# Performance work log

Hardware: AMD Instinct MI355X
Metric: run time of the kernel (lower is better)

## Reference

```python
import jax, jax.numpy as jnp
import numpy as np

B, D_MODEL, L = 4, 1024, 2048
D_STATE, D_CONV, EXPAND = 16, 4, 2
D_INNER = EXPAND * D_MODEL
DT_RANK = (D_MODEL + 15) // 16  # 64


def setup_inputs() -> dict:
    key = jax.random.key(0)
    ks = jax.random.split(key, 12)
    s = 0.02
    x = jax.random.normal(ks[0], (B, D_MODEL, L), dtype=jnp.float32)
    in_proj_w = jax.random.normal(ks[1], (2 * D_INNER, D_MODEL), dtype=jnp.float32) * s
    conv_w = jax.random.normal(ks[2], (D_INNER, D_CONV), dtype=jnp.float32) * 0.2
    conv_b = jnp.zeros((D_INNER,), dtype=jnp.float32)
    x_proj_w = jax.random.normal(ks[3], (DT_RANK + 2 * D_STATE, D_INNER), dtype=jnp.float32) * s
    dt_proj_w = jax.random.normal(ks[4], (D_INNER, DT_RANK), dtype=jnp.float32) * (DT_RANK ** -0.5)
    # bias init so softplus(bias) ~ dt in [1e-3, 1e-1], as in mamba_ssm
    dt = jnp.exp(jax.random.uniform(ks[5], (D_INNER,), dtype=jnp.float32)
                 * (np.log(0.1) - np.log(1e-3)) + np.log(1e-3))
    dt_proj_b = dt + jnp.log(-jnp.expm1(-dt))  # inverse softplus
    A_log = jnp.log(jnp.broadcast_to(jnp.arange(1, D_STATE + 1, dtype=jnp.float32),
                                     (D_INNER, D_STATE)))
    D = jnp.ones((D_INNER,), dtype=jnp.float32)
    out_proj_w = jax.random.normal(ks[6], (D_MODEL, D_INNER), dtype=jnp.float32) * s
    proj_w = jax.random.normal(ks[7], (D_MODEL, D_MODEL), dtype=jnp.float32) * s
    proj_b = jnp.zeros((D_MODEL,), dtype=jnp.float32)
    return dict(x=x, in_proj_w=in_proj_w, conv_w=conv_w, conv_b=conv_b,
                x_proj_w=x_proj_w, dt_proj_w=dt_proj_w, dt_proj_b=dt_proj_b,
                A_log=A_log, D=D, out_proj_w=out_proj_w, proj_w=proj_w, proj_b=proj_b)


def _mamba_forward(x, in_proj_w, conv_w, conv_b, x_proj_w, dt_proj_w, dt_proj_b,
                   A_log, D, out_proj_w, proj_w, proj_b):
    xt = jnp.transpose(x, (0, 2, 1))                      # (B, L, d_model)
    xz = jnp.einsum('bld,ed->ble', xt, in_proj_w)         # (B, L, 2*d_inner)
    u, z = jnp.split(xz, 2, axis=-1)                      # each (B, L, d_inner)

    # depthwise causal conv1d along time
    uc = jnp.transpose(u, (0, 2, 1))                      # (B, d_inner, L)
    upad = jnp.pad(uc, ((0, 0), (0, 0), (D_CONV - 1, 0)))
    conv = sum(conv_w[None, :, k, None] * upad[:, :, k:k + L] for k in range(D_CONV))
    conv = conv + conv_b[None, :, None]
    u = jax.nn.silu(jnp.transpose(conv, (0, 2, 1)))       # (B, L, d_inner)

    x_dbl = jnp.einsum('bld,ed->ble', u, x_proj_w)        # (B, L, dt_rank+2n)
    dt_low, Bm, Cm = jnp.split(x_dbl, [DT_RANK, DT_RANK + D_STATE], axis=-1)
    delta = jax.nn.softplus(jnp.einsum('blr,dr->bld', dt_low, dt_proj_w) + dt_proj_b)
    A = -jnp.exp(A_log)                                   # (d_inner, d_state)

    def step(h, inp):
        d_t, B_t, C_t, u_t = inp                          # (B,d),(B,n),(B,n),(B,d)
        dA = jnp.exp(d_t[:, :, None] * A[None])           # (B, d, n)
        dBu = d_t[:, :, None] * B_t[:, None, :] * u_t[:, :, None]
        h = dA * h + dBu
        y_t = jnp.einsum('bdn,bn->bd', h, C_t)
        return h, y_t

    xs = (jnp.transpose(delta, (1, 0, 2)), jnp.transpose(Bm, (1, 0, 2)),
          jnp.transpose(Cm, (1, 0, 2)), jnp.transpose(u, (1, 0, 2)))
    h0 = jnp.zeros((B, D_INNER, D_STATE), dtype=x.dtype)
    _, ys = jax.lax.scan(step, h0, xs)                    # ys: (L, B, d_inner)
    y = jnp.transpose(ys, (1, 0, 2)) + u * D              # (B, L, d_inner)
    y = y * jax.nn.silu(z)

    out = jnp.einsum('bld,ed->ble', y, out_proj_w)        # (B, L, d_model)
    out = jnp.einsum('bld,ed->ble', out, proj_w) + proj_b
    return jnp.transpose(out, (0, 2, 1))                  # (B, d_model, L)


def reference(x, in_proj_w, conv_w, conv_b, x_proj_w, dt_proj_w, dt_proj_b,
              A_log, D, out_proj_w, proj_w, proj_b):
    return _mamba_forward(x, in_proj_w, conv_w, conv_b, x_proj_w, dt_proj_w,
                          dt_proj_b, A_log, D, out_proj_w, proj_w, proj_b)
```

## Files before the change

kernel.cpp:

```cpp
#include <hip/hip_runtime.h>
#include <hip/hip_bf16.h>
#include <math.h>

#define BB 4
#define DMODEL 1024
#define LL 2048
#define DSTATE 16
#define DCONV 4
#define DINNER 2048
#define DTRANK 64
#define BL (BB * LL)
#define NCHUNK 32
#define LCH (LL / NCHUNK)
#define PFPLANE (BB * DINNER * DSTATE)
#define XPN 96
#define XPSPLIT 4
#define XPK (DINNER / XPSPLIT)

typedef unsigned short ushort;
typedef __bf16 bf16x8 __attribute__((ext_vector_type(8)));
typedef float f32x4 __attribute__((ext_vector_type(4)));

__device__ inline ushort f2bf(float f) {
    unsigned int u = __float_as_uint(f);
    u += 0x7fffu + ((u >> 16) & 1u);
    return (ushort)(u >> 16);
}
__device__ inline float bf2f(ushort h) {
    return __uint_as_float(((unsigned int)h) << 16);
}
__device__ inline float softplus_fast(float v) {
    float e = __expf(-fabsf(v));
    return fmaxf(v, 0.f) + __logf(1.f + e);
}

__device__ __forceinline__ void gload16(const ushort* g, ushort* l) {
    __builtin_amdgcn_global_load_lds(
        (__attribute__((address_space(1))) void*)g,
        (__attribute__((address_space(3))) void*)l, 16, 0, 0);
}

__global__ void f32_to_bf16(const float* __restrict__ src, ushort* __restrict__ dst, int n4) {
    int i = blockIdx.x * 256 + threadIdx.x;
    if (i < n4) {
        float4 v = ((const float4*)src)[i];
        ushort4 o;
        o.x = f2bf(v.x); o.y = f2bf(v.y); o.z = f2bf(v.z); o.w = f2bf(v.w);
        ((ushort4*)dst)[i] = o;
    }
}

__global__ void transpose_convert_x(const float* __restrict__ x, ushort* __restrict__ xtb) {
    __shared__ float tile[32][33];
    int b = blockIdx.z;
    int l0 = blockIdx.x * 32;
    int d0 = blockIdx.y * 32;
    int tx = threadIdx.x, ty = threadIdx.y;
    const float* xb = x + (size_t)b * DMODEL * LL;
#pragma unroll
    for (int j = 0; j < 32; j += 8)
        tile[ty + j][tx] = xb[(size_t)(d0 + ty + j) * LL + l0 + tx];
    __syncthreads();
    ushort* xtbb = xtb + (size_t)b * LL * DMODEL;
#pragma unroll
    for (int j = 0; j < 32; j += 8)
        xtbb[(size_t)(l0 + ty + j) * DMODEL + d0 + tx] = f2bf(tile[tx][ty + j]);
}

__global__ __launch_bounds__(256) void gemm_inproj(
    const ushort* __restrict__ A, const ushort* __restrict__ Bw,
    float* __restrict__ U, ushort* __restrict__ Z)
{
    __shared__ __align__(16) ushort As[128 * 32];
    __shared__ __align__(16) ushort Bs[128 * 32];
    const int tid = threadIdx.x;
    const int m0 = blockIdx.y * 128;
    const int n0 = blockIdx.x * 128;
    const int wave = tid >> 6;
    const int lane = tid & 63;
    const int wm = (wave >> 1) * 64;
    const int wn = (wave & 1) * 64;
    const int fr = lane & 15;
    const int fq = lane >> 4;
    const int fk = fq * 8;
    const int gr = lane >> 2;
    const int gc = (lane & 3) * 8;

    f32x4 acc[4][4];
#pragma unroll
    for (int i = 0; i < 4; ++i)
#pragma unroll
        for (int j = 0; j < 4; ++j)
            acc[i][j] = (f32x4)(0.0f);

    const ushort* Ag0 = A + (size_t)(m0 + wave * 16 + gr) * DMODEL + gc;
    const ushort* Ag1 = Ag0 + (size_t)64 * DMODEL;
    const ushort* Bg0 = Bw + (size_t)(n0 + wave * 16 + gr) * DMODEL + gc;
    const ushort* Bg1 = Bg0 + (size_t)64 * DMODEL;
    ushort* la0 = &As[wave * 512 + lane * 8];
    ushort* la1 = &As[(wave + 4) * 512 + lane * 8];
    ushort* lb0 = &Bs[wave * 512 + lane * 8];
    ushort* lb1 = &Bs[(wave + 4) * 512 + lane * 8];

    for (int k0 = 0; k0 < DMODEL; k0 += 32) {
        __syncthreads();
        gload16(Ag0 + k0, la0);
        gload16(Ag1 + k0, la1);
        gload16(Bg0 + k0, lb0);
        gload16(Bg1 + k0, lb1);
        __syncthreads();
        bf16x8 af[4], bfr[4];
#pragma unroll
        for (int i = 0; i < 4; ++i)
            af[i] = *(const bf16x8*)&As[(wm + i * 16 + fr) * 32 + fk];
#pragma unroll
        for (int j = 0; j < 4; ++j)
            bfr[j] = *(const bf16x8*)&Bs[(wn + j * 16 + fr) * 32 + fk];
#pragma unroll
        for (int i = 0; i < 4; ++i)
#pragma unroll
            for (int j = 0; j < 4; ++j)
                acc[i][j] = __builtin_amdgcn_mfma_f32_16x16x32_bf16(
                    af[i], bfr[j], acc[i][j], 0, 0, 0);
    }

    if (n0 < DINNER) {
#pragma unroll
        for (int i = 0; i < 4; ++i)
#pragma unroll
            for (int r = 0; r < 4; ++r) {
                int row = m0 + wm + i * 16 + fq * 4 + r;
#pragma unroll
                for (int j = 0; j < 4; ++j)
                    U[(size_t)row * DINNER + n0 + wn + j * 16 + fr] = acc[i][j][r];
            }
    } else {
#pragma unroll
        for (int i = 0; i < 4; ++i)
#pragma unroll
            for (int r = 0; r < 4; ++r) {
                int row = m0 + wm + i * 16 + fq * 4 + r;
#pragma unroll
                for (int j = 0; j < 4; ++j)
                    Z[(size_t)row * DINNER + (n0 - DINNER) + wn + j * 16 + fr] =
                        f2bf(acc[i][j][r]);
            }
    }
}

__global__ __launch_bounds__(256) void gemm_bf16(
    const ushort* __restrict__ A, const ushort* __restrict__ Bw,
    float* __restrict__ C, ushort* __restrict__ Cb,
    const float* __restrict__ bias,
    int M, int N, int K, int lda, int ldb, int ldc, int ldcb, int nbmax, int flags)
{
    __shared__ __align__(16) ushort As[128 * 32];
    __shared__ __align__(16) ushort Bs[128 * 32];
    const int tid = threadIdx.x;
    const int m0 = blockIdx.y * 128;
    const int n0 = blockIdx.x * 128;
    const int wave = tid >> 6;
    const int lane = tid & 63;
    const int wm = (wave >> 1) * 64;
    const int wn = (wave & 1) * 64;
    const int fr = lane & 15;
    const int fq = lane >> 4;
    const int fk = fq * 8;
    const int gr = lane >> 2;
    const int gc = (lane & 3) * 8;

    f32x4 acc[4][4];
#pragma unroll
    for (int i = 0; i < 4; ++i)
#pragma unroll
        for (int j = 0; j < 4; ++j)
            acc[i][j] = (f32x4)(0.0f);

    const ushort* Ag0 = A + (size_t)(m0 + wave * 16 + gr) * lda + gc;
    const ushort* Ag1 = Ag0 + (size_t)64 * lda;
    const ushort* Bg0 = Bw + (size_t)(n0 + wave * 16 + gr) * ldb + gc;
    const ushort* Bg1 = Bg0 + (size_t)64 * ldb;
    ushort* la0 = &As[wave * 512 + lane * 8];
    ushort* la1 = &As[(wave + 4) * 512 + lane * 8];
    ushort* lb0 = &Bs[wave * 512 + lane * 8];
    ushort* lb1 = &Bs[(wave + 4) * 512 + lane * 8];

    for (int k0 = 0; k0 < K; k0 += 32) {
        __syncthreads();
        gload16(Ag0 + k0, la0);
        gload16(Ag1 + k0, la1);
        gload16(Bg0 + k0, lb0);
        gload16(Bg1 + k0, lb1);
        __syncthreads();
        bf16x8 af[4], bfr[4];
#pragma unroll
        for (int i = 0; i < 4; ++i)
            af[i] = *(const bf16x8*)&As[(wm + i * 16 + fr) * 32 + fk];
#pragma unroll
        for (int j = 0; j < 4; ++j)
            bfr[j] = *(const bf16x8*)&Bs[(wn + j * 16 + fr) * 32 + fk];
#pragma unroll
        for (int i = 0; i < 4; ++i)
#pragma unroll
            for (int j = 0; j < 4; ++j)
                acc[i][j] = __builtin_amdgcn_mfma_f32_16x16x32_bf16(
                    af[i], bfr[j], acc[i][j], 0, 0, 0);
    }

#pragma unroll
    for (int i = 0; i < 4; ++i) {
#pragma unroll
        for (int r = 0; r < 4; ++r) {
            int row = m0 + wm + i * 16 + fq * 4 + r;
#pragma unroll
            for (int j = 0; j < 4; ++j) {
                int col = n0 + wn + j * 16 + fr;
                if (col < N) {
                    float v = acc[i][j][r];
                    if (flags & 4) v += bias[col];
                    if (flags & 8) v = softplus_fast(v);
                    if (flags & 1) C[(size_t)row * ldc + col] = v;
                    if ((flags & 2) && col < nbmax)
                        Cb[(size_t)row * ldcb + col] = f2bf(v);
                }
            }
        }
    }
}

__global__ __launch_bounds__(256) void gemm_xproj(
    const ushort* __restrict__ A, const ushort* __restrict__ Bw,
    float* __restrict__ Pp)
{
    __shared__ __align__(16) ushort As[128 * 32];
    __shared__ __align__(16) ushort Bs[128 * 32];
    const int tid = threadIdx.x;
    const int kp = blockIdx.x;
    const int m0 = blockIdx.y * 128;
    const int kbase = kp * XPK;
    const int wave = tid >> 6;
    const int lane = tid & 63;
    const int wm = (wave >> 1) * 64;
    const int wn = (wave & 1) * 64;
    const int fr = lane & 15;
    const int fq = lane >> 4;
    const int fk = fq * 8;
    const int gr = lane >> 2;
    const int gc = (lane & 3) * 8;

    f32x4 acc[4][4];
#pragma unroll
    for (int i = 0; i < 4; ++i)
#pragma unroll
        for (int j = 0; j < 4; ++j)
            acc[i][j] = (f32x4)(0.0f);

    const ushort* Ag0 = A + (size_t)(m0 + wave * 16 + gr) * DINNER + kbase + gc;
    const ushort* Ag1 = Ag0 + (size_t)64 * DINNER;
    const ushort* Bg0 = Bw + (size_t)(wave * 16 + gr) * DINNER + kbase + gc;
    const ushort* Bg1 = Bg0 + (size_t)64 * DINNER;
    ushort* la0 = &As[wave * 512 + lane * 8];
    ushort* la1 = &As[(wave + 4) * 512 + lane * 8];
    ushort* lb0 = &Bs[wave * 512 + lane * 8];
    ushort* lb1 = &Bs[(wave + 4) * 512 + lane * 8];

    for (int k0 = 0; k0 < XPK; k0 += 32) {
        __syncthreads();
        gload16(Ag0 + k0, la0);
        gload16(Ag1 + k0, la1);
        gload16(Bg0 + k0, lb0);
        gload16(Bg1 + k0, lb1);
        __syncthreads();
        bf16x8 af[4], bfr[4];
#pragma unroll
        for (int i = 0; i < 4; ++i)
            af[i] = *(const bf16x8*)&As[(wm + i * 16 + fr) * 32 + fk];
#pragma unroll
        for (int j = 0; j < 4; ++j)
            bfr[j] = *(const bf16x8*)&Bs[(wn + j * 16 + fr) * 32 + fk];
#pragma unroll
        for (int i = 0; i < 4; ++i)
#pragma unroll
            for (int j = 0; j < 4; ++j)
                acc[i][j] = __builtin_amdgcn_mfma_f32_16x16x32_bf16(
                    af[i], bfr[j], acc[i][j], 0, 0, 0);
    }

    float* Cp = Pp + (size_t)kp * ((size_t)BL * XPN);
#pragma unroll
    for (int i = 0; i < 4; ++i) {
#pragma unroll
        for (int r = 0; r < 4; ++r) {
            int row = m0 + wm + i * 16 + fq * 4 + r;
#pragma unroll
            for (int j = 0; j < 4; ++j) {
                int col = wn + j * 16 + fr;
                if (col < XPN)
                    Cp[(size_t)row * XPN + col] = acc[i][j][r];
            }
        }
    }
}

__global__ __launch_bounds__(256) void xproj_reduce(
    const float* __restrict__ Pp, float* __restrict__ xdbl, ushort* __restrict__ dtlow)
{
    int g = blockIdx.x * 256 + threadIdx.x;
    const size_t S = (size_t)BL * XPN;
    float s = (Pp[g] + Pp[g + S]) + (Pp[g + 2 * S] + Pp[g + 3 * S]);
    xdbl[g] = s;
    int row = g / XPN;
    int col = g - row * XPN;
    if (col < DTRANK) dtlow[row * DTRANK + col] = f2bf(s);
}

__global__ void conv_silu(const float* __restrict__ u, const float* __restrict__ cw,
                          const float* __restrict__ cb, ushort* __restrict__ ucb) {
    int idx = blockIdx.x * 256 + threadIdx.x;
    int d4 = idx & (DINNER / 4 - 1);
    int bl = idx >> 9;
    int l = bl & (LL - 1);
    int d = d4 << 2;
    const float* up = u + (size_t)bl * DINNER + d;
    const float4* cwv = (const float4*)cw;
    float4 w0 = cwv[d], w1 = cwv[d + 1], w2 = cwv[d + 2], w3 = cwv[d + 3];
    float4 bv = *(const float4*)(cb + d);
    float4 t = *(const float4*)(up);
    float4 a;
    a.x = fmaf(w0.w, t.x, bv.x);
    a.y = fmaf(w1.w, t.y, bv.y);
    a.z = fmaf(w2.w, t.z, bv.z);
    a.w = fmaf(w3.w, t.w, bv.w);
    if (l >= 1) {
        t = *(const float4*)(up - DINNER);
        a.x = fmaf(w0.z, t.x, a.x); a.y = fmaf(w1.z, t.y, a.y);
        a.z = fmaf(w2.z, t.z, a.z); a.w = fmaf(w3.z, t.w, a.w);
    }
    if (l >= 2) {
        t = *(const float4*)(up - 2 * DINNER);
        a.x = fmaf(w0.y, t.x, a.x); a.y = fmaf(w1.y, t.y, a.y);
        a.z = fmaf(w2.y, t.z, a.z); a.w = fmaf(w3.y, t.w, a.w);
    }
    if (l >= 3) {
        t = *(const float4*)(up - 3 * DINNER);
        a.x = fmaf(w0.x, t.x, a.x); a.y = fmaf(w1.x, t.y, a.y);
        a.z = fmaf(w2.x, t.z, a.z); a.w = fmaf(w3.x, t.w, a.w);
    }
    ushort4 o;
    o.x = f2bf(a.x / (1.f + __expf(-a.x)));
    o.y = f2bf(a.y / (1.f + __expf(-a.y)));
    o.z = f2bf(a.z / (1.f + __expf(-a.z)));
    o.w = f2bf(a.w / (1.f + __expf(-a.w)));
    ((ushort4*)ucb)[idx] = o;
}

__global__ __launch_bounds__(256) void scan_phase1(
    const ushort* __restrict__ delta16, const float* __restrict__ xdbl,
    const ushort* __restrict__ ucb, const float* __restrict__ A_log,
    float* __restrict__ P, float* __restrict__ F)
{
    int g = blockIdx.x * 256 + threadIdx.x;
    int d = g & (DINNER - 1);
    int c = (g >> 11) & (NCHUNK - 1);
    int b = g >> 16;

    float An[16], p[16], f[16];
    const float4* alp = (const float4*)(A_log + (size_t)d * DSTATE);
#pragma unroll
    for (int q = 0; q < 4; ++q) {
        float4 a = alp[q];
        An[q * 4 + 0] = -__expf(a.x); An[q * 4 + 1] = -__expf(a.y);
        An[q * 4 + 2] = -__expf(a.z); An[q * 4 + 3] = -__expf(a.w);
    }
#pragma unroll
    for (int n = 0; n < 16; ++n) { p[n] = 1.f; f[n] = 0.f; }

    size_t bl0 = (size_t)b * LL + (size_t)c * LCH;
    const ushort* dptr = delta16 + bl0 * DINNER + d;
    const ushort* uptr = ucb + bl0 * DINNER + d;
    const float* xptr = xdbl + bl0 * 96 + DTRANK;

#pragma unroll 2
    for (int l = 0; l < LCH; ++l) {
        float dv = bf2f(dptr[(size_t)l * DINNER]);
        float du = dv * bf2f(uptr[(size_t)l * DINNER]);
        float4 B0 = *(const float4*)(xptr + (size_t)l * 96);
        float4 B1 = *(const float4*)(xptr + (size_t)l * 96 + 4);
        float4 B2 = *(const float4*)(xptr + (size_t)l * 96 + 8);
        float4 B3 = *(const float4*)(xptr + (size_t)l * 96 + 12);
        float Bv[16] = {B0.x, B0.y, B0.z, B0.w, B1.x, B1.y, B1.z, B1.w,
                        B2.x, B2.y, B2.z, B2.w, B3.x, B3.y, B3.z, B3.w};
#pragma unroll
        for (int n = 0; n < 16; ++n) {
            float dA = __expf(dv * An[n]);
            f[n] = fmaf(dA, f[n], du * Bv[n]);
            p[n] *= dA;
        }
    }
    size_t o = (size_t)c * PFPLANE + ((size_t)(b * DINNER + d) << 4);
#pragma unroll
    for (int q = 0; q < 4; ++q) {
        *(float4*)(P + o + q * 4) = make_float4(p[q*4], p[q*4+1], p[q*4+2], p[q*4+3]);
        *(float4*)(F + o + q * 4) = make_float4(f[q*4], f[q*4+1], f[q*4+2], f[q*4+3]);
    }
}

__global__ __launch_bounds__(256) void scan_phase2(
    float* __restrict__ P, const float* __restrict__ F)
{
    int g = blockIdx.x * 256 + threadIdx.x;
    float h = 0.f;
#pragma unroll
    for (int c = 0; c < NCHUNK; ++c) {
        size_t idx = (size_t)c * PFPLANE + g;
        float pv = P[idx];
        float fv = F[idx];
        P[idx] = h;
        h = fmaf(pv, h, fv);
    }
}

__global__ __launch_bounds__(256) void scan_phase3(
    const ushort* __restrict__ delta16, const float* __restrict__ xdbl,
    const ushort* __restrict__ ucb, const ushort* __restrict__ zb,
    const float* __restrict__ A_log, const float* __restrict__ Dp,
    const float* __restrict__ Hin, ushort* __restrict__ ybf)
{
    int g = blockIdx.x * 256 + threadIdx.x;
    int d = g & (DINNER - 1);
    int c = (g >> 11) & (NCHUNK - 1);
    int b = g >> 16;

    float An[16], h[16];
    const float4* alp = (const float4*)(A_log + (size_t)d * DSTATE);
#pragma unroll
    for (int q = 0; q < 4; ++q) {
        float4 a = alp[q];
        An[q * 4 + 0] = -__expf(a.x); An[q * 4 + 1] = -__expf(a.y);
        An[q * 4 + 2] = -__expf(a.z); An[q * 4 + 3] = -__expf(a.w);
    }
    size_t o = (size_t)c * PFPLANE + ((size_t)(b * DINNER + d) << 4);
#pragma unroll
    for (int q = 0; q < 4; ++q) {
        float4 hv = *(const float4*)(Hin + o + q * 4);
        h[q * 4 + 0] = hv.x; h[q * 4 + 1] = hv.y;
        h[q * 4 + 2] = hv.z; h[q * 4 + 3] = hv.w;
    }
    float Dd = Dp[d];

    size_t bl0 = (size_t)b * LL + (size_t)c * LCH;
    const ushort* dptr = delta16 + bl0 * DINNER + d;
    const ushort* uptr = ucb + bl0 * DINNER + d;
    const ushort* zptr = zb + bl0 * DINNER + d;
    const float* xptr = xdbl + bl0 * 96 + DTRANK;
    ushort* yptr = ybf + bl0 * DINNER + d;

#pragma unroll 2
    for (int l = 0; l < LCH; ++l) {
        float dv = bf2f(dptr[(size_t)l * DINNER]);
        float uv = bf2f(uptr[(size_t)l * DINNER]);
        float zv = bf2f(zptr[(size_t)l * DINNER]);
        float du = dv * uv;
        float4 B0 = *(const float4*)(xptr + (size_t)l * 96);
        float4 B1 = *(const float4*)(xptr + (size_t)l * 96 + 4);
        float4 B2 = *(const float4*)(xptr + (size_t)l * 96 + 8);
        float4 B3 = *(const float4*)(xptr + (size_t)l * 96 + 12);
        float4 C0 = *(const float4*)(xptr + (size_t)l * 96 + 16);
        float4 C1 = *(const float4*)(xptr + (size_t)l * 96 + 20);
        float4 C2 = *(const float4*)(xptr + (size_t)l * 96 + 24);
        float4 C3 = *(const float4*)(xptr + (size_t)l * 96 + 28);
        float Bv[16] = {B0.x, B0.y, B0.z, B0.w, B1.x, B1.y, B1.z, B1.w,
                        B2.x, B2.y, B2.z, B2.w, B3.x, B3.y, B3.z, B3.w};
        float Cv[16] = {C0.x, C0.y, C0.z, C0.w, C1.x, C1.y, C1.z, C1.w,
                        C2.x, C2.y, C2.z, C2.w, C3.x, C3.y, C3.z, C3.w};
        float y0 = 0.f, y1 = 0.f, y2 = 0.f, y3 = 0.f;
#pragma unroll
        for (int n = 0; n < 4; ++n) {
            float dA0 = __expf(dv * An[n]);
            float dA1 = __expf(dv * An[n + 4]);
            float dA2 = __expf(dv * An[n + 8]);
            float dA3 = __expf(dv * An[n + 12]);
            h[n]      = fmaf(dA0, h[n],      du * Bv[n]);
            h[n + 4]  = fmaf(dA1, h[n + 4],  du * Bv[n + 4]);
            h[n + 8]  = fmaf(dA2, h[n + 8],  du * Bv[n + 8]);
            h[n + 12] = fmaf(dA3, h[n + 12], du * Bv[n + 12]);
            y0 = fmaf(h[n],      Cv[n],      y0);
            y1 = fmaf(h[n + 4],  Cv[n + 4],  y1);
            y2 = fmaf(h[n + 8],  Cv[n + 8],  y2);
            y3 = fmaf(h[n + 12], Cv[n + 12], y3);
        }
        float y = (y0 + y1) + (y2 + y3);
        float sz = zv / (1.f + __expf(-zv));
        yptr[(size_t)l * DINNER] = f2bf((y + uv * Dd) * sz);
    }
}

__global__ void transpose_out(const float* __restrict__ o2, float* __restrict__ out) {
    __shared__ float tile[32][33];
    int b = blockIdx.z;
    int l0 = blockIdx.x * 32;
    int e0 = blockIdx.y * 32;
    int tx = threadIdx.x, ty = threadIdx.y;
    const float* ob = o2 + (size_t)b * LL * DMODEL;
#pragma unroll
    for (int j = 0; j < 32; j += 8)
        tile[ty + j][tx] = ob[(size_t)(l0 + ty + j) * DMODEL + e0 + tx];
    __syncthreads();
    float* outb = out + (size_t)b * DMODEL * LL;
#pragma unroll
    for (int j = 0; j < 32; j += 8)
        outb[(size_t)(e0 + ty + j) * LL + l0 + tx] = tile[tx][ty + j];
}

extern "C" void kernel_launch(void* const* d_in, const int* in_sizes, int n_in,
                              void* d_out, int out_size, void* d_ws, size_t ws_size,
                              hipStream_t stream) {
    const float* x         = (const float*)d_in[0];
    const float* in_proj_w = (const float*)d_in[1];
    const float* conv_w    = (const float*)d_in[2];
    const float* conv_b    = (const float*)d_in[3];
    const float* x_proj_w  = (const float*)d_in[4];
    const float* dt_proj_w = (const float*)d_in[5];
    const float* dt_proj_b = (const float*)d_in[6];
    const float* A_log     = (const float*)d_in[7];
    const float* Dp        = (const float*)d_in[8];
    const float* out_proj_w= (const float*)d_in[9];
    const float* proj_w    = (const float*)d_in[10];
    const float* proj_b    = (const float*)d_in[11];
    float* out = (float*)d_out;

    char* wsb = (char*)d_ws;
    float*  bufU    = (float*)(wsb);
    ushort* delta16 = (ushort*)(wsb);
    float*  Pbuf    = (float*)(wsb + ((size_t)32 << 20));
    float*  xprojP  = (float*)(wsb + ((size_t)32 << 20));
    float*  Fbuf    = (float*)(wsb + ((size_t)48 << 20));
    ushort* zb      = (ushort*)(wsb + ((size_t)64 << 20));
    ushort* xtb     = (ushort*)(wsb + ((size_t)96 << 20));
    ushort* ucb     = (ushort*)(wsb + ((size_t)96 << 20));
    ushort* ybf     = (ushort*)(wsb + ((size_t)128 << 20));
    float*  xdbl    = (float*)(wsb + ((size_t)160 << 20));
    ushort* dtlow   = (ushort*)(wsb + ((size_t)163 << 20));
    ushort* wip     = (ushort*)(wsb + ((size_t)164 << 20));
    ushort* wxp     = wip + (size_t)4194304;
    ushort* wdt     = wxp + (size_t)196608;
    ushort* wop     = wdt + (size_t)131072;
    ushort* wpj     = wop + (size_t)2097152;
    float*  out2    = (float*)(wsb);
    ushort* out1b   = (ushort*)(wsb + ((size_t)32 << 20));

    f32_to_bf16<<<dim3(4096), 256, 0, stream>>>(in_proj_w, wip, 1048576);
    f32_to_bf16<<<dim3(192),  256, 0, stream>>>(x_proj_w,  wxp, 49152);
    f32_to_bf16<<<dim3(128),  256, 0, stream>>>(dt_proj_w, wdt, 32768);
    f32_to_bf16<<<dim3(2048), 256, 0, stream>>>(out_proj_w, wop, 524288);
    f32_to_bf16<<<dim3(1024), 256, 0, stream>>>(proj_w,    wpj, 262144);

    transpose_convert_x<<<dim3(LL / 32, DMODEL / 32, BB), dim3(32, 8), 0, stream>>>(x, xtb);

    gemm_inproj<<<dim3(2 * DINNER / 128, BL / 128), 256, 0, stream>>>(
        xtb, wip, bufU, zb);

    conv_silu<<<dim3(BL * DINNER / 4 / 256), 256, 0, stream>>>(bufU, conv_w, conv_b, ucb);

    gemm_xproj<<<dim3(XPSPLIT, BL / 128), 256, 0, stream>>>(ucb, wxp, xprojP);
    xproj_reduce<<<dim3(BL * XPN / 256), 256, 0, stream>>>(xprojP, xdbl, dtlow);

    gemm_bf16<<<dim3(DINNER / 128, BL / 128), 256, 0, stream>>>(
        dtlow, wdt, nullptr, delta16, dt_proj_b,
        BL, DINNER, DTRANK, DTRANK, DTRANK, 0, DINNER, DINNER, 2 | 4 | 8);

    const int scan_threads = BB * NCHUNK * DINNER;
    scan_phase1<<<dim3(scan_threads / 256), 256, 0, stream>>>(
        delta16, xdbl, ucb, A_log, Pbuf, Fbuf);
    scan_phase2<<<dim3(PFPLANE / 256), 256, 0, stream>>>(Pbuf, Fbuf);
    scan_phase3<<<dim3(scan_threads / 256), 256, 0, stream>>>(
        delta16, xdbl, ucb, zb, A_log, Dp, Pbuf, ybf);

    gemm_bf16<<<dim3(DMODEL / 128, BL / 128), 256, 0, stream>>>(
        ybf, wop, nullptr, out1b, nullptr,
        BL, DMODEL, DINNER, DINNER, DINNER, 0, DMODEL, DMODEL, 2);

    gemm_bf16<<<dim3(DMODEL / 128, BL / 128), 256, 0, stream>>>(
        out1b, wpj, out2, nullptr, proj_b,
        BL, DMODEL, DMODEL, DMODEL, DMODEL, DMODEL, 0, 0, 1 | 4);

    transpose_out<<<dim3(LL / 32, DMODEL / 32, BB), dim3(32, 8), 0, stream>>>(out2, out);
}
```

Before: 649.4 us.

## Double-buffer LDS in GEMMs and fuse output transpose into final projection

All three bf16 GEMM kernels now use two LDS buffers so the global-to-LDS load of the next k-tile is issued before the MFMAs on the current tile, with one barrier per iteration instead of two. The final projection GEMM is computed with swapped operands (weights times activations), so its epilogue writes directly into the (B, d_model, L) output layout with a per-row bias, and the separate transpose kernel and its intermediate buffer are removed. This doubles LDS usage per block, which may lower occupancy. The transposed-layout stores are strided along L per lane group and may coalesce less well.

```diff
diff --git a/kernel.cpp b/kernel.cpp
--- a/kernel.cpp
+++ b/kernel.cpp
@@ -67,12 +67,13 @@
         xtbb[(size_t)(l0 + ty + j) * DMODEL + d0 + tx] = f2bf(tile[tx][ty + j]);
 }
 
+
 __global__ __launch_bounds__(256) void gemm_inproj(
     const ushort* __restrict__ A, const ushort* __restrict__ Bw,
     float* __restrict__ U, ushort* __restrict__ Z)
 {
-    __shared__ __align__(16) ushort As[128 * 32];
-    __shared__ __align__(16) ushort Bs[128 * 32];
+    __shared__ __align__(16) ushort As[2][128 * 32];
+    __shared__ __align__(16) ushort Bs[2][128 * 32];
     const int tid = threadIdx.x;
     const int m0 = blockIdx.y * 128;
     const int n0 = blockIdx.x * 128;
@@ -97,31 +98,39 @@
     const ushort* Ag1 = Ag0 + (size_t)64 * DMODEL;
     const ushort* Bg0 = Bw + (size_t)(n0 + wave * 16 + gr) * DMODEL + gc;
     const ushort* Bg1 = Bg0 + (size_t)64 * DMODEL;
-    ushort* la0 = &As[wave * 512 + lane * 8];
-    ushort* la1 = &As[(wave + 4) * 512 + lane * 8];
-    ushort* lb0 = &Bs[wave * 512 + lane * 8];
-    ushort* lb1 = &Bs[(wave + 4) * 512 + lane * 8];
-
-    for (int k0 = 0; k0 < DMODEL; k0 += 32) {
-        __syncthreads();
-        gload16(Ag0 + k0, la0);
-        gload16(Ag1 + k0, la1);
-        gload16(Bg0 + k0, lb0);
-        gload16(Bg1 + k0, lb1);
-        __syncthreads();
+
+    auto stage = [&](int s, int k0) {
+        gload16(Ag0 + k0, &As[s][wave * 512 + lane * 8]);
+        gload16(Ag1 + k0, &As[s][(wave + 4) * 512 + lane * 8]);
+        gload16(Bg0 + k0, &Bs[s][wave * 512 + lane * 8]);
+        gload16(Bg1 + k0, &Bs[s][(wave + 4) * 512 + lane * 8]);
+    };
+
+    stage(0, 0);
+    asm volatile("s_waitcnt vmcnt(0)" ::: "memory");
+    __builtin_amdgcn_s_barrier();
+    asm volatile("" ::: "memory");
+
+    const int NT = DMODEL / 32;
+    for (int t = 0; t < NT; ++t) {
+        const int cur = t & 1;
+        if (t + 1 < NT) stage(cur ^ 1, (t + 1) * 32);
         bf16x8 af[4], bfr[4];
 #pragma unroll
         for (int i = 0; i < 4; ++i)
-            af[i] = *(const bf16x8*)&As[(wm + i * 16 + fr) * 32 + fk];
+            af[i] = *(const bf16x8*)&As[cur][(wm + i * 16 + fr) * 32 + fk];
 #pragma unroll
         for (int j = 0; j < 4; ++j)
-            bfr[j] = *(const bf16x8*)&Bs[(wn + j * 16 + fr) * 32 + fk];
+            bfr[j] = *(const bf16x8*)&Bs[cur][(wn + j * 16 + fr) * 32 + fk];
 #pragma unroll
         for (int i = 0; i < 4; ++i)
 #pragma unroll
             for (int j = 0; j < 4; ++j)
                 acc[i][j] = __builtin_amdgcn_mfma_f32_16x16x32_bf16(
                     af[i], bfr[j], acc[i][j], 0, 0, 0);
+        asm volatile("s_waitcnt vmcnt(0) lgkmcnt(0)" ::: "memory");
+        __builtin_amdgcn_s_barrier();
+        asm volatile("" ::: "memory");
     }
 
     if (n0 < DINNER) {
@@ -154,8 +163,8 @@
     const float* __restrict__ bias,
     int M, int N, int K, int lda, int ldb, int ldc, int ldcb, int nbmax, int flags)
 {
-    __shared__ __align__(16) ushort As[128 * 32];
-    __shared__ __align__(16) ushort Bs[128 * 32];
+    __shared__ __align__(16) ushort As[2][128 * 32];
+    __shared__ __align__(16) ushort Bs[2][128 * 32];
     const int tid = threadIdx.x;
     const int m0 = blockIdx.y * 128;
     const int n0 = blockIdx.x * 128;
@@ -180,31 +189,39 @@
     const ushort* Ag1 = Ag0 + (size_t)64 * lda;
     const ushort* Bg0 = Bw + (size_t)(n0 + wave * 16 + gr) * ldb + gc;
     const ushort* Bg1 = Bg0 + (size_t)64 * ldb;
-    ushort* la0 = &As[wave * 512 + lane * 8];
-    ushort* la1 = &As[(wave + 4) * 512 + lane * 8];
-    ushort* lb0 = &Bs[wave * 512 + lane * 8];
-    ushort* lb1 = &Bs[(wave + 4) * 512 + lane * 8];
-
-    for (int k0 = 0; k0 < K; k0 += 32) {
-        __syncthreads();
-        gload16(Ag0 + k0, la0);
-        gload16(Ag1 + k0, la1);
-        gload16(Bg0 + k0, lb0);
-        gload16(Bg1 + k0, lb1);
-        __syncthreads();
+
+    auto stage = [&](int s, int k0) {
+        gload16(Ag0 + k0, &As[s][wave * 512 + lane * 8]);
+        gload16(Ag1 + k0, &As[s][(wave + 4) * 512 + lane * 8]);
+        gload16(Bg0 + k0, &Bs[s][wave * 512 + lane * 8]);
+        gload16(Bg1 + k0, &Bs[s][(wave + 4) * 512 + lane * 8]);
+    };
+
+    stage(0, 0);
+    asm volatile("s_waitcnt vmcnt(0)" ::: "memory");
+    __builtin_amdgcn_s_barrier();
+    asm volatile("" ::: "memory");
+
+    const int NT = K / 32;
+    for (int t = 0; t < NT; ++t) {
+        const int cur = t & 1;
+        if (t + 1 < NT) stage(cur ^ 1, (t + 1) * 32);
         bf16x8 af[4], bfr[4];
 #pragma unroll
         for (int i = 0; i < 4; ++i)
-            af[i] = *(const bf16x8*)&As[(wm + i * 16 + fr) * 32 + fk];
+            af[i] = *(const bf16x8*)&As[cur][(wm + i * 16 + fr) * 32 + fk];
 #pragma unroll
         for (int j = 0; j < 4; ++j)
-            bfr[j] = *(const bf16x8*)&Bs[(wn + j * 16 + fr) * 32 + fk];
+            bfr[j] = *(const bf16x8*)&Bs[cur][(wn + j * 16 + fr) * 32 + fk];
 #pragma unroll
         for (int i = 0; i < 4; ++i)
 #pragma unroll
             for (int j = 0; j < 4; ++j)
                 acc[i][j] = __builtin_amdgcn_mfma_f32_16x16x32_bf16(
                     af[i], bfr[j], acc[i][j], 0, 0, 0);
+        asm volatile("s_waitcnt vmcnt(0) lgkmcnt(0)" ::: "memory");
+        __builtin_amdgcn_s_barrier();
+        asm volatile("" ::: "memory");
     }
 
 #pragma unroll
@@ -217,11 +234,18 @@
                 int col = n0 + wn + j * 16 + fr;
                 if (col < N) {
                     float v = acc[i][j][r];
-                    if (flags & 4) v += bias[col];
-                    if (flags & 8) v = softplus_fast(v);
-                    if (flags & 1) C[(size_t)row * ldc + col] = v;
-                    if ((flags & 2) && col < nbmax)
-                        Cb[(size_t)row * ldcb + col] = f2bf(v);
+                    if (flags & 16) {
+                        v += bias[row];
+                        int bq = col >> 11;
+                        int l  = col & (LL - 1);
+                        C[(size_t)bq * DMODEL * LL + (size_t)row * LL + l] = v;
+                    } else {
+                        if (flags & 4) v += bias[col];
+                        if (flags & 8) v = softplus_fast(v);
+                        if (flags & 1) C[(size_t)row * ldc + col] = v;
+                        if ((flags & 2) && col < nbmax)
+                            Cb[(size_t)row * ldcb + col] = f2bf(v);
+                    }
                 }
             }
         }
@@ -232,8 +256,8 @@
     const ushort* __restrict__ A, const ushort* __restrict__ Bw,
     float* __restrict__ Pp)
 {
-    __shared__ __align__(16) ushort As[128 * 32];
-    __shared__ __align__(16) ushort Bs[128 * 32];
+    __shared__ __align__(16) ushort As[2][128 * 32];
+    __shared__ __align__(16) ushort Bs[2][128 * 32];
     const int tid = threadIdx.x;
     const int kp = blockIdx.x;
     const int m0 = blockIdx.y * 128;
@@ -259,31 +283,39 @@
     const ushort* Ag1 = Ag0 + (size_t)64 * DINNER;
     const ushort* Bg0 = Bw + (size_t)(wave * 16 + gr) * DINNER + kbase + gc;
     const ushort* Bg1 = Bg0 + (size_t)64 * DINNER;
-    ushort* la0 = &As[wave * 512 + lane * 8];
-    ushort* la1 = &As[(wave + 4) * 512 + lane * 8];
-    ushort* lb0 = &Bs[wave * 512 + lane * 8];
-    ushort* lb1 = &Bs[(wave + 4) * 512 + lane * 8];
-
-    for (int k0 = 0; k0 < XPK; k0 += 32) {
-        __syncthreads();
-        gload16(Ag0 + k0, la0);
-        gload16(Ag1 + k0, la1);
-        gload16(Bg0 + k0, lb0);
-        gload16(Bg1 + k0, lb1);
-        __syncthreads();
+
+    auto stage = [&](int s, int k0) {
+        gload16(Ag0 + k0, &As[s][wave * 512 + lane * 8]);
+        gload16(Ag1 + k0, &As[s][(wave + 4) * 512 + lane * 8]);
+        gload16(Bg0 + k0, &Bs[s][wave * 512 + lane * 8]);
+        gload16(Bg1 + k0, &Bs[s][(wave + 4) * 512 + lane * 8]);
+    };
+
+    stage(0, 0);
+    asm volatile("s_waitcnt vmcnt(0)" ::: "memory");
+    __builtin_amdgcn_s_barrier();
+    asm volatile("" ::: "memory");
+
+    const int NT = XPK / 32;
+    for (int t = 0; t < NT; ++t) {
+        const int cur = t & 1;
+        if (t + 1 < NT) stage(cur ^ 1, (t + 1) * 32);
         bf16x8 af[4], bfr[4];
 #pragma unroll
         for (int i = 0; i < 4; ++i)
-            af[i] = *(const bf16x8*)&As[(wm + i * 16 + fr) * 32 + fk];
+            af[i] = *(const bf16x8*)&As[cur][(wm + i * 16 + fr) * 32 + fk];
 #pragma unroll
         for (int j = 0; j < 4; ++j)
-            bfr[j] = *(const bf16x8*)&Bs[(wn + j * 16 + fr) * 32 + fk];
+            bfr[j] = *(const bf16x8*)&Bs[cur][(wn + j * 16 + fr) * 32 + fk];
 #pragma unroll
         for (int i = 0; i < 4; ++i)
 #pragma unroll
             for (int j = 0; j < 4; ++j)
                 acc[i][j] = __builtin_amdgcn_mfma_f32_16x16x32_bf16(
                     af[i], bfr[j], acc[i][j], 0, 0, 0);
+        asm volatile("s_waitcnt vmcnt(0) lgkmcnt(0)" ::: "memory");
+        __builtin_amdgcn_s_barrier();
+        asm volatile("" ::: "memory");
     }
 
     float* Cp = Pp + (size_t)kp * ((size_t)BL * XPN);
@@ -495,23 +527,6 @@
     }
 }
 
-__global__ void transpose_out(const float* __restrict__ o2, float* __restrict__ out) {
-    __shared__ float tile[32][33];
-    int b = blockIdx.z;
-    int l0 = blockIdx.x * 32;
-    int e0 = blockIdx.y * 32;
-    int tx = threadIdx.x, ty = threadIdx.y;
-    const float* ob = o2 + (size_t)b * LL * DMODEL;
-#pragma unroll
-    for (int j = 0; j < 32; j += 8)
-        tile[ty + j][tx] = ob[(size_t)(l0 + ty + j) * DMODEL + e0 + tx];
-    __syncthreads();
-    float* outb = out + (size_t)b * DMODEL * LL;
-#pragma unroll
-    for (int j = 0; j < 32; j += 8)
-        outb[(size_t)(e0 + ty + j) * LL + l0 + tx] = tile[tx][ty + j];
-}
-
 extern "C" void kernel_launch(void* const* d_in, const int* in_sizes, int n_in,
                               void* d_out, int out_size, void* d_ws, size_t ws_size,
                               hipStream_t stream) {
@@ -546,7 +561,6 @@
     ushort* wdt     = wxp + (size_t)196608;
     ushort* wop     = wdt + (size_t)131072;
     ushort* wpj     = wop + (size_t)2097152;
-    float*  out2    = (float*)(wsb);
     ushort* out1b   = (ushort*)(wsb + ((size_t)32 << 20));
 
     f32_to_bf16<<<dim3(4096), 256, 0, stream>>>(in_proj_w, wip, 1048576);
@@ -580,9 +594,7 @@
         ybf, wop, nullptr, out1b, nullptr,
         BL, DMODEL, DINNER, DINNER, DINNER, 0, DMODEL, DMODEL, 2);
 
-    gemm_bf16<<<dim3(DMODEL / 128, BL / 128), 256, 0, stream>>>(
-        out1b, wpj, out2, nullptr, proj_b,
-        BL, DMODEL, DMODEL, DMODEL, DMODEL, DMODEL, 0, 0, 1 | 4);
-
-    transpose_out<<<dim3(LL / 32, DMODEL / 32, BB), dim3(32, 8), 0, stream>>>(out2, out);
-}
+    gemm_bf16<<<dim3(BL / 128, DMODEL / 128), 256, 0, stream>>>(
+        wpj, out1b, out, nullptr, proj_b,
+        DMODEL, BL, DMODEL, DMODEL, DMODEL, 0, 0, 0, 16);
+}
```

Measured after the change: 620.2 us. 1.05x faster.
